# Kernel tuning notes

Measured on AMD Instinct MI355X. Metric: run time of the kernel, lower is better.

## Reference

```python
import jax, jax.numpy as jnp
import numpy as np

PI = 3.1415926
EPS_LN = 1e-5
SLOPE = 0.01  # nn.LeakyReLU default negative_slope


def _leaky(x):
    return jnp.where(x >= 0, x, SLOPE * x)


def _layernorm(x):
    # normalizes over dims (1,2) of [B,C,L], biased variance
    mean = x.mean(axis=(1, 2), keepdims=True)
    var = x.var(axis=(1, 2), keepdims=True)
    return (x - mean) / jnp.sqrt(var + EPS_LN)


def _conv1d(x, w, b):
    # x [B,C,L], w [O,I,3]
    y = jax.lax.conv_general_dilated(x, w, window_strides=(1,), padding='SAME',
                                     dimension_numbers=('NCH', 'OIH', 'NCH'))
    return y + b[None, :, None]


def _conv_stack(x, w1, b1, w2, b2, w3, b3):
    x = _leaky(_layernorm(_conv1d(x, w1, b1)))
    x = _leaky(_layernorm(_conv1d(x, w2, b2)))
    x = _leaky(_layernorm(_conv1d(x, w3, b3)))
    return x


def _context_pooling(feats, w1, b1, w2, b2, w3, b3, r=0.1):
    # feats [B,L,D]
    B, L, D = feats.shape
    sw = _conv_stack(feats.transpose(0, 2, 1), w1, b1, w2, b2, w3, b3)  # [B,2,L]
    s = jax.nn.softmax(sw[:, 0, :], axis=1)  # [B,L]
    w = jax.nn.softmax(sw[:, 1, :], axis=1)  # [B,L]
    std = r * L * s  # [B,L] (per query/center i)
    pos = jnp.arange(L, dtype=feats.dtype)
    diff2 = (pos[None, :] - pos[:, None]) ** 2  # [Li,Lj], (place - center)^2
    g = (2 * PI) ** -0.5 * (std[:, :, None] ** -1) * jnp.exp(
        -diff2[None] / (1e-5 + 2.0 * std[:, :, None] ** 2))  # [B,Li,Lj]
    g = g / jnp.max(g, axis=2, keepdims=True)
    W = g * w[:, None, :]  # [B,Li,Lj]
    return jnp.einsum('bij,bjd->bid', W, feats)


def setup_inputs() -> dict:
    key = jax.random.key(0)
    ks = jax.random.split(key, 16)
    B, L, D = 16, 1024, 640
    D2 = 2 * D
    f32 = jnp.float32
    sc = 0.02
    inp = {
        'feats': jax.random.normal(ks[0], (B, L, D), f32),
        # ContextPooling conv stack
        'cp_w1': jax.random.normal(ks[1], (D2, D, 3), f32) * sc,
        'cp_b1': jnp.zeros((D2,), f32),
        'cp_w2': jax.random.normal(ks[2], (D2, D2, 3), f32) * sc,
        'cp_b2': jnp.zeros((D2,), f32),
        'cp_w3': jax.random.normal(ks[3], (2, D2, 3), f32) * sc,
        'cp_b3': jnp.zeros((2,), f32),
        # SoluModel conv stack
        'cv_w1': jax.random.normal(ks[4], (D2, D, 3), f32) * sc,
        'cv_b1': jnp.zeros((D2,), f32),
        'cv_w2': jax.random.normal(ks[5], (D2, D2, 3), f32) * sc,
        'cv_b2': jnp.zeros((D2,), f32),
        'cv_w3': jax.random.normal(ks[6], (D, D2, 3), f32) * sc,
        'cv_b3': jnp.zeros((D,), f32),
        # MLP: Linear(2D -> D), torch init normal(0, 0.01), bias 0
        'mlp_w': jax.random.normal(ks[7], (D, 2 * D), f32) * 0.01,
        'mlp_b': jnp.zeros((D,), f32),
    }
    return inp


def reference(feats, cp_w1, cp_b1, cp_w2, cp_b2, cp_w3, cp_b3,
              cv_w1, cv_b1, cv_w2, cv_b2, cv_w3, cv_b3, mlp_w, mlp_b):
    out_sa = _context_pooling(feats, cp_w1, cp_b1, cp_w2, cp_b2, cp_w3, cp_b3) + feats
    out_conv = _conv_stack(feats.transpose(0, 2, 1),
                           cv_w1, cv_b1, cv_w2, cv_b2, cv_w3, cv_b3)
    out_conv = out_conv.transpose(0, 2, 1) + feats
    out = jnp.concatenate([out_sa, out_conv], axis=2)  # [B,L,2D]
    # Dropout(p=0.6) is identity at inference
    out = _leaky(jnp.einsum('bld,od->blo', out, mlp_w) + mlp_b)
    return out
```

## Files before the change

kernel.cpp:

```cpp
#include <hip/hip_runtime.h>
#include <hip/hip_bf16.h>
#include <math.h>

#define SLOPE 0.01f
#define EPS_LN 1e-5f

typedef __hip_bfloat16 bf16;
typedef __attribute__((ext_vector_type(8))) short short8;
typedef __attribute__((ext_vector_type(4))) float f32x4;

__device__ __forceinline__ float leakyf(float x) { return x < 0.f ? SLOPE * x : x; }

__device__ __forceinline__ float b2f(short s) {
    unsigned u = ((unsigned)(unsigned short)s) << 16;
    return __builtin_bit_cast(float, u);
}
__device__ __forceinline__ short f2b(float f) {
    __hip_bfloat16 h = __float2bfloat16(f);
    return *(short*)&h;
}

__device__ __forceinline__ void gload_lds16(const void* g, void* l) {
    __builtin_amdgcn_global_load_lds(
        (const __attribute__((address_space(1))) void*)g,
        (__attribute__((address_space(3))) void*)l, 16, 0, 0);
}

template <int EPI>
__global__ __launch_bounds__(256, 2) void gemm_bf16(
    const bf16* __restrict__ A, long sA, int ldA,
    const bf16* __restrict__ Bt,
    const float* __restrict__ bias,
    void* __restrict__ Outv, long sO, int ldO, int K,
    int gx, int gy, float2* __restrict__ stats)
{
    __shared__ bf16 As[128][64];
    __shared__ bf16 Bs[128][64];

    const int nwg = gridDim.x;
    const int wid = (blockIdx.x & 7) * (nwg >> 3) + (blockIdx.x >> 3);
    const int bx = wid % gx;
    const int by = (wid / gx) % gy;
    const int bz = wid / (gx * gy);

    const bf16* Ab = A + (long)bz * sA + (long)by * 128 * ldA;
    const bf16* Bb = Bt + (long)bx * 128 * K;
    const int tid = threadIdx.x;
    const int wave = tid >> 6, lane = tid & 63;
    const int moff = (wave >> 1) * 64, noff = (wave & 1) * 64;
    const int r16 = lane & 15, g4 = lane >> 4;
    const int r7 = r16 & 7;

    f32x4 acc[4][4];
#pragma unroll
    for (int i = 0; i < 4; ++i)
#pragma unroll
        for (int j = 0; j < 4; ++j)
            acc[i][j] = (f32x4){0.f, 0.f, 0.f, 0.f};

    for (int k0 = 0; k0 < K; k0 += 64) {
        __syncthreads();
#pragma unroll
        for (int i = 0; i < 4; ++i) {
            int chunk = i * 256 + tid;
            int row = chunk >> 3;
            int kc = (chunk ^ (chunk >> 3)) & 7;
            gload_lds16(Ab + (long)row * ldA + (k0 + kc * 8),
                        (char*)(&As[0][0]) + (i * 256 + wave * 64) * 16);
        }
#pragma unroll
        for (int i = 0; i < 4; ++i) {
            int chunk = i * 256 + tid;
            int row = chunk >> 3;
            int kc = (chunk ^ (chunk >> 3)) & 7;
            gload_lds16(Bb + (long)row * K + (k0 + kc * 8),
                        (char*)(&Bs[0][0]) + (i * 256 + wave * 64) * 16);
        }
        __syncthreads();
#pragma unroll
        for (int kk = 0; kk < 2; ++kk) {
            short8 af[4], bfr[4];
#pragma unroll
            for (int mi = 0; mi < 4; ++mi)
                af[mi] = *(const short8*)&As[moff + mi * 16 + r16][((kk * 4 + g4) ^ r7) * 8];
#pragma unroll
            for (int ni = 0; ni < 4; ++ni)
                bfr[ni] = *(const short8*)&Bs[noff + ni * 16 + r16][((kk * 4 + g4) ^ r7) * 8];
#pragma unroll
            for (int mi = 0; mi < 4; ++mi)
#pragma unroll
                for (int ni = 0; ni < 4; ++ni)
                    acc[mi][ni] = __builtin_amdgcn_mfma_f32_16x16x32_bf16(
                        af[mi], bfr[ni], acc[mi][ni], 0, 0, 0);
        }
    }

    float s = 0.f, q = 0.f;
#pragma unroll
    for (int mi = 0; mi < 4; ++mi) {
#pragma unroll
        for (int ni = 0; ni < 4; ++ni) {
            int col = bx * 128 + noff + ni * 16 + r16;
            float bv = bias[col];
#pragma unroll
            for (int r = 0; r < 4; ++r) {
                int row = by * 128 + moff + mi * 16 + g4 * 4 + r;
                float v = acc[mi][ni][r] + bv;
                if (EPI == 1) {
                    ((float*)Outv)[(long)bz * sO + (long)row * ldO + col] = leakyf(v);
                } else {
                    ((bf16*)Outv)[(long)bz * sO + (long)row * ldO + col] = __float2bfloat16(v);
                    s += v; q += v * v;
                }
            }
        }
    }
    if (EPI == 0) {
        __syncthreads();
        float* red = (float*)&As[0][0];
        float* red2 = red + 256;
        red[tid] = s; red2[tid] = q;
        __syncthreads();
        for (int o = 128; o; o >>= 1) {
            if (tid < o) { red[tid] += red[tid + o]; red2[tid] += red2[tid + o]; }
            __syncthreads();
        }
        if (tid == 0) {
            atomicAdd(&stats[bz].x, red[0]);
            atomicAdd(&stats[bz].y, red2[0]);
        }
    }
}

__global__ void zero_stats_k(float2* s) {
    if (threadIdx.x < 16) s[threadIdx.x] = make_float2(0.f, 0.f);
}

__global__ void fin_k(const float2* __restrict__ acc, float2* __restrict__ stat, float invN) {
    int b = threadIdx.x;
    if (b < 16) {
        float m = acc[b].x * invN;
        float var = acc[b].y * invN - m * m;
        stat[b] = make_float2(m, rsqrtf(var + EPS_LN));
    }
}

__global__ void pack_feats_v_k(const float* __restrict__ f, bf16* __restrict__ xp, int C)
{
    long i8 = (long)blockIdx.x * 256 + threadIdx.x;
    long total8 = 16L * 1026 * C / 8;
    if (i8 >= total8) return;
    long e = i8 * 8;
    int c = (int)(e % C);
    long t = e / C;
    int r = (int)(t % 1026);
    int b = (int)(t / 1026);
    short8 o;
    if (r == 0 || r == 1025) {
#pragma unroll
        for (int j = 0; j < 8; ++j) o[j] = 0;
    } else {
        const float* src = f + ((long)b * 1024 + (r - 1)) * C + c;
        f32x4 v0 = *(const f32x4*)src;
        f32x4 v1 = *(const f32x4*)(src + 4);
#pragma unroll
        for (int j = 0; j < 4; ++j) { o[j] = f2b(v0[j]); o[j + 4] = f2b(v1[j]); }
    }
    *(short8*)(xp + e) = o;
}

__global__ void norm_pack_v_k(const bf16* __restrict__ y, const float2* __restrict__ stat,
                              bf16* __restrict__ xp, int C)
{
    long i8 = (long)blockIdx.x * 256 + threadIdx.x;
    long total8 = 16L * 1026 * C / 8;
    if (i8 >= total8) return;
    long e = i8 * 8;
    int c = (int)(e % C);
    long t = e / C;
    int r = (int)(t % 1026);
    int b = (int)(t / 1026);
    short8 o;
    if (r == 0 || r == 1025) {
#pragma unroll
        for (int j = 0; j < 8; ++j) o[j] = 0;
    } else {
        float2 st = stat[b];
        short8 v = *(const short8*)(y + ((long)b * 1024 + (r - 1)) * C + c);
#pragma unroll
        for (int j = 0; j < 8; ++j)
            o[j] = f2b(leakyf((b2f(v[j]) - st.x) * st.y));
    }
    *(short8*)(xp + e) = o;
}

__global__ void norm_addf_v_k(const bf16* __restrict__ y, const float2* __restrict__ stat,
                              const float* __restrict__ feats, bf16* __restrict__ acat)
{
    long i8 = (long)blockIdx.x * 256 + threadIdx.x;
    long total8 = 16L * 1024 * 640 / 8;
    if (i8 >= total8) return;
    long e = i8 * 8;
    int c = (int)(e % 640);
    int l = (int)((e / 640) % 1024);
    int b = (int)(e / (640L * 1024));
    float2 st = stat[b];
    short8 v = *(const short8*)(y + e);
    f32x4 f0 = *(const f32x4*)(feats + e);
    f32x4 f1 = *(const f32x4*)(feats + e + 4);
    short8 o;
#pragma unroll
    for (int j = 0; j < 4; ++j) {
        o[j] = f2b(leakyf((b2f(v[j]) - st.x) * st.y) + f0[j]);
        o[j + 4] = f2b(leakyf((b2f(v[j + 4]) - st.x) * st.y) + f1[j]);
    }
    *(short8*)(acat + ((long)b * 1024 + l) * 1280 + 640 + c) = o;
}

__global__ void conv3cp_k(const bf16* __restrict__ xp, const bf16* __restrict__ w3,
                          const float* __restrict__ b3, float* __restrict__ sw)
{
    int wid = (int)((blockIdx.x * 256 + threadIdx.x) >> 6);
    int lane = threadIdx.x & 63;
    int b = wid >> 10, l = wid & 1023;
    const bf16* xr = xp + ((long)b * 1026 + l) * 1280;
    float a0 = 0.f, a1 = 0.f;
    for (int k = lane; k < 3840; k += 64) {
        float x = __bfloat162float(xr[k]);
        a0 += x * __bfloat162float(w3[k]);
        a1 += x * __bfloat162float(w3[3840 + k]);
    }
    for (int o = 32; o; o >>= 1) { a0 += __shfl_down(a0, o); a1 += __shfl_down(a1, o); }
    if (lane == 0) {
        sw[b * 2048 + l] = a0 + b3[0];
        sw[b * 2048 + 1024 + l] = a1 + b3[1];
    }
}

__global__ __launch_bounds__(256) void cp_post_k(const float* __restrict__ sw,
                                                 float* __restrict__ stdb,
                                                 float* __restrict__ wb)
{
    int b = blockIdx.x, tid = threadIdx.x;
    __shared__ float s0[1024], s1[1024], red[256];
    const float* p = sw + b * 2048;
    float s = 0.f, q = 0.f;
    for (int l = tid; l < 1024; l += 256) {
        float v0 = p[l], v1 = p[1024 + l];
        s0[l] = v0; s1[l] = v1;
        s += v0 + v1; q += v0 * v0 + v1 * v1;
    }
    red[tid] = s; __syncthreads();
    for (int o = 128; o; o >>= 1) { if (tid < o) red[tid] += red[tid + o]; __syncthreads(); }
    float mean = red[0] / 2048.f; __syncthreads();
    red[tid] = q; __syncthreads();
    for (int o = 128; o; o >>= 1) { if (tid < o) red[tid] += red[tid + o]; __syncthreads(); }
    float inv = rsqrtf(red[0] / 2048.f - mean * mean + EPS_LN); __syncthreads();
    for (int l = tid; l < 1024; l += 256) {
        s0[l] = leakyf((s0[l] - mean) * inv);
        s1[l] = leakyf((s1[l] - mean) * inv);
    }
    __syncthreads();
    float mx = -1e30f;
    for (int l = tid; l < 1024; l += 256) mx = fmaxf(mx, s0[l]);
    red[tid] = mx; __syncthreads();
    for (int o = 128; o; o >>= 1) { if (tid < o) red[tid] = fmaxf(red[tid], red[tid + o]); __syncthreads(); }
    mx = red[0]; __syncthreads();
    float se = 0.f;
    for (int l = tid; l < 1024; l += 256) { float e = __expf(s0[l] - mx); s0[l] = e; se += e; }
    red[tid] = se; __syncthreads();
    for (int o = 128; o; o >>= 1) { if (tid < o) red[tid] += red[tid + o]; __syncthreads(); }
    float rs = 1.f / red[0]; __syncthreads();
    for (int l = tid; l < 1024; l += 256) stdb[b * 1024 + l] = 102.4f * s0[l] * rs;
    mx = -1e30f;
    for (int l = tid; l < 1024; l += 256) mx = fmaxf(mx, s1[l]);
    red[tid] = mx; __syncthreads();
    for (int o = 128; o; o >>= 1) { if (tid < o) red[tid] = fmaxf(red[tid], red[tid + o]); __syncthreads(); }
    mx = red[0]; __syncthreads();
    se = 0.f;
    for (int l = tid; l < 1024; l += 256) { float e = __expf(s1[l] - mx); s1[l] = e; se += e; }
    red[tid] = se; __syncthreads();
    for (int o = 128; o; o >>= 1) { if (tid < o) red[tid] += red[tid + o]; __syncthreads(); }
    rs = 1.f / red[0]; __syncthreads();
    for (int l = tid; l < 1024; l += 256) wb[b * 1024 + l] = s1[l] * rs;
}

__global__ __launch_bounds__(256) void pool_k(const float* __restrict__ feats,
                                              const float* __restrict__ stdb,
                                              const float* __restrict__ wb,
                                              bf16* __restrict__ acat)
{
    int i = blockIdx.x, b = blockIdx.y, tid = threadIdx.x;
    float sd = stdb[b * 1024 + i];
    float den = 1e-5f + 2.f * sd * sd;
    float inv = 1.f / den;
    int R = (int)sqrtf(11.5129255f * den) + 1;
    int jlo = max(0, i - R), jhi = min(1023, i + R);
    __shared__ float cj[256];
    float a0 = 0.f, a1 = 0.f, a2 = 0.f;
    const float* fb = feats + (long)b * 1024 * 640;
    for (int j0 = jlo; j0 <= jhi; j0 += 256) {
        int j = j0 + tid;
        float c = 0.f;
        if (j <= jhi) {
            float d = (float)(j - i);
            c = __expf(-d * d * inv) * wb[b * 1024 + j];
        }
        __syncthreads();
        cj[tid] = c;
        __syncthreads();
        int lim = min(256, jhi - j0 + 1);
        for (int t = 0; t < lim; ++t) {
            float cc = cj[t];
            const float* fr = fb + (long)(j0 + t) * 640;
            a0 += cc * fr[tid];
            a1 += cc * fr[tid + 256];
            if (tid < 128) a2 += cc * fr[tid + 512];
        }
    }
    long obase = ((long)b * 1024 + i) * 1280;
    long fbase = ((long)b * 1024 + i) * 640;
    acat[obase + tid] = __float2bfloat16(a0 + feats[fbase + tid]);
    acat[obase + tid + 256] = __float2bfloat16(a1 + feats[fbase + tid + 256]);
    if (tid < 128) acat[obase + tid + 512] = __float2bfloat16(a2 + feats[fbase + tid + 512]);
}

__global__ void repack_w_k(const float* __restrict__ w, bf16* __restrict__ bt, int CO, int CI)
{
    long idx = (long)blockIdx.x * 256 + threadIdx.x;
    long total = (long)CO * CI * 3;
    if (idx >= total) return;
    int K3 = 3 * CI;
    int o = (int)(idx / K3);
    int k = (int)(idx % K3);
    int t = k / CI, ci = k % CI;
    bt[idx] = __float2bfloat16(w[(long)o * CI * 3 + ci * 3 + t]);
}

__global__ void cast_bf16_k(const float* __restrict__ w, bf16* __restrict__ o, long n)
{
    long idx = (long)blockIdx.x * 256 + threadIdx.x;
    if (idx < n) o[idx] = __float2bfloat16(w[idx]);
}

extern "C" void kernel_launch(void* const* d_in, const int* in_sizes, int n_in,
                              void* d_out, int out_size, void* d_ws, size_t ws_size,
                              hipStream_t stream)
{
    const float* feats = (const float*)d_in[0];
    const float* cp_w1 = (const float*)d_in[1];
    const float* cp_b1 = (const float*)d_in[2];
    const float* cp_w2 = (const float*)d_in[3];
    const float* cp_b2 = (const float*)d_in[4];
    const float* cp_w3 = (const float*)d_in[5];
    const float* cp_b3 = (const float*)d_in[6];
    const float* cv_w1 = (const float*)d_in[7];
    const float* cv_b1 = (const float*)d_in[8];
    const float* cv_w2 = (const float*)d_in[9];
    const float* cv_b2 = (const float*)d_in[10];
    const float* cv_w3 = (const float*)d_in[11];
    const float* cv_b3 = (const float*)d_in[12];
    const float* mlp_w = (const float*)d_in[13];
    const float* mlp_b = (const float*)d_in[14];
    float* out = (float*)d_out;

    char* ws = (char*)d_ws;
    size_t off = 0;
    auto alloc = [&](size_t bytes) -> char* {
        char* p = ws + off;
        off += (bytes + 255) & ~(size_t)255;
        return p;
    };
    bf16* XpadF = (bf16*)alloc(16L * 1026 * 640 * 2);
    bf16* Xpad2 = (bf16*)alloc(16L * 1026 * 1280 * 2);
    bf16* Ybf = (bf16*)alloc(16L * 1024 * 1280 * 2);
    bf16* Acat = (bf16*)alloc(16L * 1024 * 1280 * 2);
    bf16* Bcp1 = (bf16*)alloc(1280L * 1920 * 2);
    bf16* Bcp2 = (bf16*)alloc(1280L * 3840 * 2);
    bf16* Bcp3 = (bf16*)alloc(2L * 3840 * 2);
    bf16* Bcv1 = (bf16*)alloc(1280L * 1920 * 2);
    bf16* Bcv2 = (bf16*)alloc(1280L * 3840 * 2);
    bf16* Bcv3 = (bf16*)alloc(640L * 3840 * 2);
    bf16* Bmlp = (bf16*)alloc(640L * 1280 * 2);
    float* swb = (float*)alloc(16L * 2048 * 4);
    float* stdb = (float*)alloc(16L * 1024 * 4);
    float* wbf = (float*)alloc(16L * 1024 * 4);
    float2* sacc = (float2*)alloc(16L * 8);
    float2* stat = (float2*)alloc(16L * 8);
    (void)ws_size; (void)in_sizes; (void)n_in; (void)out_size;

    const long NF8 = 16L * 1026 * 640 / 8;
    const long N28 = 16L * 1026 * 1280 / 8;
    const long NA8 = 16L * 1024 * 640 / 8;
    const long N1280 = 1024L * 1280, N640 = 1024L * 640;
    const float inv1280 = 1.f / (float)N1280, inv640 = 1.f / (float)N640;

    pack_feats_v_k<<<(NF8 + 255) / 256, 256, 0, stream>>>(feats, XpadF, 640);
    repack_w_k<<<(1280L * 640 * 3 + 255) / 256, 256, 0, stream>>>(cp_w1, Bcp1, 1280, 640);
    repack_w_k<<<(1280L * 1280 * 3 + 255) / 256, 256, 0, stream>>>(cp_w2, Bcp2, 1280, 1280);
    repack_w_k<<<(2L * 1280 * 3 + 255) / 256, 256, 0, stream>>>(cp_w3, Bcp3, 2, 1280);
    repack_w_k<<<(1280L * 640 * 3 + 255) / 256, 256, 0, stream>>>(cv_w1, Bcv1, 1280, 640);
    repack_w_k<<<(1280L * 1280 * 3 + 255) / 256, 256, 0, stream>>>(cv_w2, Bcv2, 1280, 1280);
    repack_w_k<<<(640L * 1280 * 3 + 255) / 256, 256, 0, stream>>>(cv_w3, Bcv3, 640, 1280);
    cast_bf16_k<<<(640L * 1280 + 255) / 256, 256, 0, stream>>>(mlp_w, Bmlp, 640L * 1280);

    zero_stats_k<<<1, 64, 0, stream>>>(sacc);
    gemm_bf16<0><<<1280, 256, 0, stream>>>(XpadF, 1026L * 640, 640, Bcp1, cp_b1,
                                           Ybf, N1280, 1280, 1920, 10, 8, sacc);
    fin_k<<<1, 64, 0, stream>>>(sacc, stat, inv1280);
    norm_pack_v_k<<<(N28 + 255) / 256, 256, 0, stream>>>(Ybf, stat, Xpad2, 1280);
    zero_stats_k<<<1, 64, 0, stream>>>(sacc);
    gemm_bf16<0><<<1280, 256, 0, stream>>>(Xpad2, 1026L * 1280, 1280, Bcp2, cp_b2,
                                           Ybf, N1280, 1280, 3840, 10, 8, sacc);
    fin_k<<<1, 64, 0, stream>>>(sacc, stat, inv1280);
    norm_pack_v_k<<<(N28 + 255) / 256, 256, 0, stream>>>(Ybf, stat, Xpad2, 1280);
    conv3cp_k<<<4096, 256, 0, stream>>>(Xpad2, Bcp3, cp_b3, swb);
    cp_post_k<<<16, 256, 0, stream>>>(swb, stdb, wbf);
    pool_k<<<dim3(1024, 16), 256, 0, stream>>>(feats, stdb, wbf, Acat);

    zero_stats_k<<<1, 64, 0, stream>>>(sacc);
    gemm_bf16<0><<<1280, 256, 0, stream>>>(XpadF, 1026L * 640, 640, Bcv1, cv_b1,
                                           Ybf, N1280, 1280, 1920, 10, 8, sacc);
    fin_k<<<1, 64, 0, stream>>>(sacc, stat, inv1280);
    norm_pack_v_k<<<(N28 + 255) / 256, 256, 0, stream>>>(Ybf, stat, Xpad2, 1280);
    zero_stats_k<<<1, 64, 0, stream>>>(sacc);
    gemm_bf16<0><<<1280, 256, 0, stream>>>(Xpad2, 1026L * 1280, 1280, Bcv2, cv_b2,
                                           Ybf, N1280, 1280, 3840, 10, 8, sacc);
    fin_k<<<1, 64, 0, stream>>>(sacc, stat, inv1280);
    norm_pack_v_k<<<(N28 + 255) / 256, 256, 0, stream>>>(Ybf, stat, Xpad2, 1280);
    zero_stats_k<<<1, 64, 0, stream>>>(sacc);
    gemm_bf16<0><<<640, 256, 0, stream>>>(Xpad2, 1026L * 1280, 1280, Bcv3, cv_b3,
                                          Ybf, N640, 640, 3840, 5, 8, sacc);
    fin_k<<<1, 64, 0, stream>>>(sacc, stat, inv640);
    norm_addf_v_k<<<(NA8 + 255) / 256, 256, 0, stream>>>(Ybf, stat, feats, Acat);

    gemm_bf16<1><<<640, 256, 0, stream>>>(Acat, N1280, 1280, Bmlp, mlp_b,
                                          out, N640, 640, 1280, 5, 8, nullptr);
}
```

Measured before the change: 855.3 us.

## Batch paired conv-stack GEMMs into a 256x256-tile 8-wave pipelined kernel

Adds a new 512-thread GEMM kernel with 256x256 tiles, four-slot LDS ring buffering via direct global-to-LDS loads, XOR-swizzled LDS layout, and explicit barrier/priority scheduling around MFMA phases. The ContextPooling and conv-stack first and second layers, which share shapes, now run as single launches covering both branches, each keeping its own stats slots. This removes launch and tail overhead and gives larger tiles more operand reuse. It also vectorizes the conv3cp dot product with 16-byte loads and aliases workspace buffers. The cost is more buffers, heavy register use at one block per CU, and dependence on hand-tuned waitcnt counts.

```diff
diff --git a/kernel.cpp b/kernel.cpp
--- a/kernel.cpp
+++ b/kernel.cpp
@@ -24,6 +24,162 @@
     __builtin_amdgcn_global_load_lds(
         (const __attribute__((address_space(1))) void*)g,
         (__attribute__((address_space(3))) void*)l, 16, 0, 0);
+}
+
+#define PHASE_MFMA(NFB)                                                        \
+    asm volatile("s_barrier" ::: "memory");                                    \
+    asm volatile("s_waitcnt lgkmcnt(0)" ::: "memory");                         \
+    __builtin_amdgcn_sched_barrier(0);                                         \
+    __builtin_amdgcn_s_setprio(1);                                             \
+    _Pragma("unroll")                                                          \
+    for (int mi = 0; mi < 8; ++mi) {                                           \
+        acc[mi][NFB] = __builtin_amdgcn_mfma_f32_16x16x32_bf16(                \
+            areg[mi], b0, acc[mi][NFB], 0, 0, 0);                              \
+        acc[mi][NFB + 1] = __builtin_amdgcn_mfma_f32_16x16x32_bf16(            \
+            areg[mi], b1, acc[mi][NFB + 1], 0, 0, 0);                          \
+    }                                                                          \
+    __builtin_amdgcn_s_setprio(0);
+
+template <int MODE>
+__global__ __launch_bounds__(512, 1) void gemm8_bf16(
+    const bf16* __restrict__ A0, const bf16* __restrict__ A1,
+    const bf16* __restrict__ Bt0, const bf16* __restrict__ Bt1,
+    const float* __restrict__ bias0, const float* __restrict__ bias1,
+    bf16* __restrict__ Y0, bf16* __restrict__ Y1,
+    float2* __restrict__ sacc)
+{
+    constexpr int K   = (MODE == 0) ? 1920 : 3840;
+    constexpr int LDA = (MODE == 0) ? 640 : 1280;
+    constexpr int MT  = (MODE == 0) ? 64 : 128;
+    constexpr int NKT = K / 64;
+
+    __shared__ bf16 Ash[4][256][32];
+    __shared__ bf16 Bsh[4][256][32];
+
+    const int nwg = gridDim.x;
+    const int wid = (blockIdx.x & 7) * (nwg >> 3) + (blockIdx.x >> 3);
+    const int mt = wid % MT;
+    const int bxg = wid / MT;
+    int branch, bxl, mtl;
+    if (MODE == 0) { branch = bxg >= 5; bxl = bxg - branch * 5; mtl = mt; }
+    else           { branch = mt >= 64; bxl = bxg; mtl = mt & 63; }
+    const int batch = mtl >> 2;
+    const int mrow0 = (mtl & 3) * 256;
+    const bf16* Apad = branch ? A1 : A0;
+    const bf16* Bt   = branch ? Bt1 : Bt0;
+    const float* bias = branch ? bias1 : bias0;
+    bf16* Yb = branch ? Y1 : Y0;
+    const bf16* Abase = Apad + ((long)batch * 1026 + mrow0) * LDA;
+    const bf16* Bbase = Bt + (long)bxl * 256 * K;
+
+    const int tid = threadIdx.x;
+    const int wave = tid >> 6, lane = tid & 63;
+    const int wm = wave >> 2, wn = wave & 3;
+    const int r16 = lane & 15, g4 = lane >> 4;
+
+    auto stageA = [&](int s, int kh) {
+        char* lb = (char*)&Ash[(2 * s + kh) & 3][0][0];
+#pragma unroll
+        for (int j = 0; j < 2; ++j) {
+            int c = j * 512 + tid;
+            int L = c ^ ((c >> 3) & 7);
+            int row = L >> 2, kg = L & 3;
+            gload_lds16(Abase + (long)row * LDA + (s * 64 + kh * 32 + kg * 8),
+                        lb + c * 16);
+        }
+    };
+    auto stageB = [&](int s, int kh) {
+        char* lb = (char*)&Bsh[(2 * s + kh) & 3][0][0];
+#pragma unroll
+        for (int j = 0; j < 2; ++j) {
+            int c = j * 512 + tid;
+            int L = c ^ ((c >> 3) & 7);
+            int row = L >> 2, kg = L & 3;
+            gload_lds16(Bbase + (long)row * K + (s * 64 + kh * 32 + kg * 8),
+                        lb + c * 16);
+        }
+    };
+    auto ldA8 = [&](int reg, int mi) -> short8 {
+        int row = wm * 128 + mi * 16 + r16;
+        int P = ((row << 2) | g4) ^ ((row >> 1) & 7);
+        return *(const short8*)((const char*)&Ash[reg][0][0] + P * 16);
+    };
+    auto ldB8 = [&](int reg, int q) -> short8 {
+        int row = wn * 64 + q * 16 + r16;
+        int P = ((row << 2) | g4) ^ ((row >> 1) & 7);
+        return *(const short8*)((const char*)&Bsh[reg][0][0] + P * 16);
+    };
+
+    f32x4 acc[8][4];
+#pragma unroll
+    for (int i = 0; i < 8; ++i)
+#pragma unroll
+        for (int j = 0; j < 4; ++j) acc[i][j] = (f32x4){0.f, 0.f, 0.f, 0.f};
+
+    stageA(0, 0); stageB(0, 0);
+    stageA(0, 1); stageB(0, 1);
+    stageA(1, 0); stageB(1, 0);
+    asm volatile("s_waitcnt vmcnt(8)" ::: "memory");
+    asm volatile("s_barrier" ::: "memory");
+
+    short8 areg[8];
+    short8 b0, b1;
+    for (int s = 0; s < NKT; ++s) {
+        const int rA = (2 * s) & 3;
+        const int rB = (2 * s + 1) & 3;
+#pragma unroll
+        for (int mi = 0; mi < 8; ++mi) areg[mi] = ldA8(rA, mi);
+        b0 = ldB8(rA, 0); b1 = ldB8(rA, 1);
+        if (s + 1 < NKT) stageA(s + 1, 1);
+        PHASE_MFMA(0)
+        asm volatile("s_barrier" ::: "memory");
+        b0 = ldB8(rA, 2); b1 = ldB8(rA, 3);
+        if (s + 1 < NKT) stageB(s + 1, 1);
+        PHASE_MFMA(2)
+        asm volatile("s_waitcnt vmcnt(8)" ::: "memory");
+        asm volatile("s_barrier" ::: "memory");
+#pragma unroll
+        for (int mi = 0; mi < 8; ++mi) areg[mi] = ldA8(rB, mi);
+        b0 = ldB8(rB, 0); b1 = ldB8(rB, 1);
+        if (s + 2 < NKT) stageA(s + 2, 0);
+        PHASE_MFMA(0)
+        asm volatile("s_barrier" ::: "memory");
+        b0 = ldB8(rB, 2); b1 = ldB8(rB, 3);
+        if (s + 2 < NKT) stageB(s + 2, 0);
+        PHASE_MFMA(2)
+        asm volatile("s_waitcnt vmcnt(8)" ::: "memory");
+        asm volatile("s_barrier" ::: "memory");
+    }
+    asm volatile("s_waitcnt vmcnt(0) lgkmcnt(0)" ::: "memory");
+
+    float ssum = 0.f, sq = 0.f;
+#pragma unroll
+    for (int mi = 0; mi < 8; ++mi) {
+#pragma unroll
+        for (int q = 0; q < 4; ++q) {
+            int col = bxl * 256 + wn * 64 + q * 16 + r16;
+            float bv = bias[col];
+#pragma unroll
+            for (int rr = 0; rr < 4; ++rr) {
+                int row = mrow0 + wm * 128 + mi * 16 + g4 * 4 + rr;
+                float v = acc[mi][q][rr] + bv;
+                Yb[((long)batch * 1024 + row) * 1280 + col] = __float2bfloat16(v);
+                ssum += v; sq += v * v;
+            }
+        }
+    }
+    __syncthreads();
+    float* red = (float*)&Ash[0][0][0];
+    red[tid] = ssum; red[512 + tid] = sq;
+    __syncthreads();
+    for (int o = 256; o; o >>= 1) {
+        if (tid < o) { red[tid] += red[tid + o]; red[512 + tid] += red[512 + tid + o]; }
+        __syncthreads();
+    }
+    if (tid == 0) {
+        atomicAdd(&sacc[branch * 16 + batch].x, red[0]);
+        atomicAdd(&sacc[branch * 16 + batch].y, red[512]);
+    }
 }
 
 template <int EPI>
@@ -133,12 +289,13 @@
 }
 
 __global__ void zero_stats_k(float2* s) {
-    if (threadIdx.x < 16) s[threadIdx.x] = make_float2(0.f, 0.f);
-}
-
-__global__ void fin_k(const float2* __restrict__ acc, float2* __restrict__ stat, float invN) {
+    if (threadIdx.x < 80) s[threadIdx.x] = make_float2(0.f, 0.f);
+}
+
+__global__ void fin_k(const float2* __restrict__ acc, float2* __restrict__ stat,
+                      float invN, int n) {
     int b = threadIdx.x;
-    if (b < 16) {
+    if (b < n) {
         float m = acc[b].x * invN;
         float var = acc[b].y * invN - m * m;
         stat[b] = make_float2(m, rsqrtf(var + EPS_LN));
@@ -223,12 +380,18 @@
     int wid = (int)((blockIdx.x * 256 + threadIdx.x) >> 6);
     int lane = threadIdx.x & 63;
     int b = wid >> 10, l = wid & 1023;
-    const bf16* xr = xp + ((long)b * 1026 + l) * 1280;
+    const short8* xr = (const short8*)(xp + ((long)b * 1026 + l) * 1280);
+    const short8* w0 = (const short8*)w3;
+    const short8* w1 = (const short8*)(w3 + 3840);
     float a0 = 0.f, a1 = 0.f;
-    for (int k = lane; k < 3840; k += 64) {
-        float x = __bfloat162float(xr[k]);
-        a0 += x * __bfloat162float(w3[k]);
-        a1 += x * __bfloat162float(w3[3840 + k]);
+    for (int c = lane; c < 480; c += 64) {
+        short8 x = xr[c], u = w0[c], v = w1[c];
+#pragma unroll
+        for (int j = 0; j < 8; ++j) {
+            float xf = b2f(x[j]);
+            a0 += xf * b2f(u[j]);
+            a1 += xf * b2f(v[j]);
+        }
     }
     for (int o = 32; o; o >>= 1) { a0 += __shfl_down(a0, o); a1 += __shfl_down(a1, o); }
     if (lane == 0) {
@@ -371,22 +534,25 @@
         off += (bytes + 255) & ~(size_t)255;
         return p;
     };
-    bf16* XpadF = (bf16*)alloc(16L * 1026 * 640 * 2);
-    bf16* Xpad2 = (bf16*)alloc(16L * 1026 * 1280 * 2);
-    bf16* Ybf = (bf16*)alloc(16L * 1024 * 1280 * 2);
-    bf16* Acat = (bf16*)alloc(16L * 1024 * 1280 * 2);
-    bf16* Bcp1 = (bf16*)alloc(1280L * 1920 * 2);
+    char* R1 = alloc(16L * 1024 * 1280 * 2);
+    bf16* XpadF = (bf16*)R1;
+    bf16* Acat = (bf16*)R1;
+    bf16* Xp_cp = (bf16*)alloc(16L * 1026 * 1280 * 2);
+    bf16* Xp_cv = (bf16*)alloc(16L * 1026 * 1280 * 2);
+    bf16* Y0 = (bf16*)alloc(16L * 1024 * 1280 * 2);
+    bf16* Y1 = (bf16*)alloc(16L * 1024 * 1280 * 2);
+    bf16* Ycv3 = Y0;
+    bf16* Bm1 = (bf16*)alloc(2560L * 1920 * 2);
     bf16* Bcp2 = (bf16*)alloc(1280L * 3840 * 2);
+    bf16* Bcv2 = (bf16*)alloc(1280L * 3840 * 2);
     bf16* Bcp3 = (bf16*)alloc(2L * 3840 * 2);
-    bf16* Bcv1 = (bf16*)alloc(1280L * 1920 * 2);
-    bf16* Bcv2 = (bf16*)alloc(1280L * 3840 * 2);
     bf16* Bcv3 = (bf16*)alloc(640L * 3840 * 2);
     bf16* Bmlp = (bf16*)alloc(640L * 1280 * 2);
     float* swb = (float*)alloc(16L * 2048 * 4);
     float* stdb = (float*)alloc(16L * 1024 * 4);
     float* wbf = (float*)alloc(16L * 1024 * 4);
-    float2* sacc = (float2*)alloc(16L * 8);
-    float2* stat = (float2*)alloc(16L * 8);
+    float2* sacc = (float2*)alloc(80L * 8);
+    float2* stat = (float2*)alloc(80L * 8);
     (void)ws_size; (void)in_sizes; (void)n_in; (void)out_size;
 
     const long NF8 = 16L * 1026 * 640 / 8;
@@ -395,44 +561,36 @@
     const long N1280 = 1024L * 1280, N640 = 1024L * 640;
     const float inv1280 = 1.f / (float)N1280, inv640 = 1.f / (float)N640;
 
+    zero_stats_k<<<1, 128, 0, stream>>>(sacc);
     pack_feats_v_k<<<(NF8 + 255) / 256, 256, 0, stream>>>(feats, XpadF, 640);
-    repack_w_k<<<(1280L * 640 * 3 + 255) / 256, 256, 0, stream>>>(cp_w1, Bcp1, 1280, 640);
+    repack_w_k<<<(1280L * 640 * 3 + 255) / 256, 256, 0, stream>>>(cp_w1, Bm1, 1280, 640);
+    repack_w_k<<<(1280L * 640 * 3 + 255) / 256, 256, 0, stream>>>(cv_w1, Bm1 + 1280L * 1920, 1280, 640);
     repack_w_k<<<(1280L * 1280 * 3 + 255) / 256, 256, 0, stream>>>(cp_w2, Bcp2, 1280, 1280);
+    repack_w_k<<<(1280L * 1280 * 3 + 255) / 256, 256, 0, stream>>>(cv_w2, Bcv2, 1280, 1280);
     repack_w_k<<<(2L * 1280 * 3 + 255) / 256, 256, 0, stream>>>(cp_w3, Bcp3, 2, 1280);
-    repack_w_k<<<(1280L * 640 * 3 + 255) / 256, 256, 0, stream>>>(cv_w1, Bcv1, 1280, 640);
-    repack_w_k<<<(1280L * 1280 * 3 + 255) / 256, 256, 0, stream>>>(cv_w2, Bcv2, 1280, 1280);
     repack_w_k<<<(640L * 1280 * 3 + 255) / 256, 256, 0, stream>>>(cv_w3, Bcv3, 640, 1280);
     cast_bf16_k<<<(640L * 1280 + 255) / 256, 256, 0, stream>>>(mlp_w, Bmlp, 640L * 1280);
 
-    zero_stats_k<<<1, 64, 0, stream>>>(sacc);
-    gemm_bf16<0><<<1280, 256, 0, stream>>>(XpadF, 1026L * 640, 640, Bcp1, cp_b1,
-                                           Ybf, N1280, 1280, 1920, 10, 8, sacc);
-    fin_k<<<1, 64, 0, stream>>>(sacc, stat, inv1280);
-    norm_pack_v_k<<<(N28 + 255) / 256, 256, 0, stream>>>(Ybf, stat, Xpad2, 1280);
-    zero_stats_k<<<1, 64, 0, stream>>>(sacc);
-    gemm_bf16<0><<<1280, 256, 0, stream>>>(Xpad2, 1026L * 1280, 1280, Bcp2, cp_b2,
-                                           Ybf, N1280, 1280, 3840, 10, 8, sacc);
-    fin_k<<<1, 64, 0, stream>>>(sacc, stat, inv1280);
-    norm_pack_v_k<<<(N28 + 255) / 256, 256, 0, stream>>>(Ybf, stat, Xpad2, 1280);
-    conv3cp_k<<<4096, 256, 0, stream>>>(Xpad2, Bcp3, cp_b3, swb);
+    gemm8_bf16<0><<<640, 512, 0, stream>>>(XpadF, XpadF, Bm1, Bm1 + 1280L * 1920,
+                                           cp_b1, cv_b1, Y0, Y1, sacc);
+    fin_k<<<1, 64, 0, stream>>>(sacc, stat, inv1280, 32);
+    norm_pack_v_k<<<(N28 + 255) / 256, 256, 0, stream>>>(Y0, stat, Xp_cp, 1280);
+    norm_pack_v_k<<<(N28 + 255) / 256, 256, 0, stream>>>(Y1, stat + 16, Xp_cv, 1280);
+
+    gemm8_bf16<1><<<640, 512, 0, stream>>>(Xp_cp, Xp_cv, Bcp2, Bcv2,
+                                           cp_b2, cv_b2, Y0, Y1, sacc + 32);
+    fin_k<<<1, 64, 0, stream>>>(sacc + 32, stat + 32, inv1280, 32);
+    norm_pack_v_k<<<(N28 + 255) / 256, 256, 0, stream>>>(Y0, stat + 32, Xp_cp, 1280);
+    norm_pack_v_k<<<(N28 + 255) / 256, 256, 0, stream>>>(Y1, stat + 48, Xp_cv, 1280);
+
+    conv3cp_k<<<4096, 256, 0, stream>>>(Xp_cp, Bcp3, cp_b3, swb);
     cp_post_k<<<16, 256, 0, stream>>>(swb, stdb, wbf);
     pool_k<<<dim3(1024, 16), 256, 0, stream>>>(feats, stdb, wbf, Acat);
 
-    zero_stats_k<<<1, 64, 0, stream>>>(sacc);
-    gemm_bf16<0><<<1280, 256, 0, stream>>>(XpadF, 1026L * 640, 640, Bcv1, cv_b1,
-                                           Ybf, N1280, 1280, 1920, 10, 8, sacc);
-    fin_k<<<1, 64, 0, stream>>>(sacc, stat, inv1280);
-    norm_pack_v_k<<<(N28 + 255) / 256, 256, 0, stream>>>(Ybf, stat, Xpad2, 1280);
-    zero_stats_k<<<1, 64, 0, stream>>>(sacc);
-    gemm_bf16<0><<<1280, 256, 0, stream>>>(Xpad2, 1026L * 1280, 1280, Bcv2, cv_b2,
-                                           Ybf, N1280, 1280, 3840, 10, 8, sacc);
-    fin_k<<<1, 64, 0, stream>>>(sacc, stat, inv1280);
-    norm_pack_v_k<<<(N28 + 255) / 256, 256, 0, stream>>>(Ybf, stat, Xpad2, 1280);
-    zero_stats_k<<<1, 64, 0, stream>>>(sacc);
-    gemm_bf16<0><<<640, 256, 0, stream>>>(Xpad2, 1026L * 1280, 1280, Bcv3, cv_b3,
-                                          Ybf, N640, 640, 3840, 5, 8, sacc);
-    fin_k<<<1, 64, 0, stream>>>(sacc, stat, inv640);
-    norm_addf_v_k<<<(NA8 + 255) / 256, 256, 0, stream>>>(Ybf, stat, feats, Acat);
+    gemm_bf16<0><<<640, 256, 0, stream>>>(Xp_cv, 1026L * 1280, 1280, Bcv3, cv_b3,
+                                          Ycv3, N640, 640, 3840, 5, 8, sacc + 64);
+    fin_k<<<1, 64, 0, stream>>>(sacc + 64, stat + 64, inv640, 16);
+    norm_addf_v_k<<<(NA8 + 255) / 256, 256, 0, stream>>>(Ycv3, stat + 64, feats, Acat);
 
     gemm_bf16<1><<<640, 256, 0, stream>>>(Acat, N1280, 1280, Bmlp, mlp_b,
                                           out, N640, 640, 1280, 5, 8, nullptr);
```

Measured after the change: 910.1 us. +6.4%, slower.

## Batch context-pooling and conv branches into dual GEMM launches

Applied to the files above, without the earlier changes.

Merges the matching layer-1 and layer-2 convolution GEMMs of the two branches into single launches with twice the workgroups. Each workgroup picks its branch pointers, and each branch gets separate stats slots, all zeroed once. The workspace is reorganised so both branches keep their own intermediate buffers, and the input pack buffer is aliased with the concat buffer. Separately, the final 2-channel conv is vectorised to 16-byte loads. This targets launch overhead and wave tail inefficiency, at the cost of more workspace.

```diff
diff --git a/kernel.cpp b/kernel.cpp
--- a/kernel.cpp
+++ b/kernel.cpp
@@ -27,21 +27,30 @@
 }
 
 template <int EPI>
-__global__ __launch_bounds__(256, 2) void gemm_bf16(
-    const bf16* __restrict__ A, long sA, int ldA,
-    const bf16* __restrict__ Bt,
-    const float* __restrict__ bias,
-    void* __restrict__ Outv, long sO, int ldO, int K,
-    int gx, int gy, float2* __restrict__ stats)
+__global__ __launch_bounds__(256, 2) void gemm_dual(
+    const bf16* __restrict__ A0, const bf16* __restrict__ A1, long sA, int ldA,
+    const bf16* __restrict__ Bt0, const bf16* __restrict__ Bt1,
+    const float* __restrict__ bias0, const float* __restrict__ bias1,
+    void* __restrict__ Out0, void* __restrict__ Out1, long sO, int ldO, int K,
+    int gx, int gy, int halfwg,
+    float2* __restrict__ stats0, float2* __restrict__ stats1)
 {
     __shared__ bf16 As[128][64];
     __shared__ bf16 Bs[128][64];
 
     const int nwg = gridDim.x;
     const int wid = (blockIdx.x & 7) * (nwg >> 3) + (blockIdx.x >> 3);
-    const int bx = wid % gx;
-    const int by = (wid / gx) % gy;
-    const int bz = wid / (gx * gy);
+    const int branch = wid >= halfwg;
+    const int w = wid - branch * halfwg;
+    const int bx = w % gx;
+    const int by = (w / gx) % gy;
+    const int bz = w / (gx * gy);
+
+    const bf16* A = branch ? A1 : A0;
+    const bf16* Bt = branch ? Bt1 : Bt0;
+    const float* bias = branch ? bias1 : bias0;
+    void* Outv = branch ? Out1 : Out0;
+    float2* stats = branch ? stats1 : stats0;
 
     const bf16* Ab = A + (long)bz * sA + (long)by * 128 * ldA;
     const bf16* Bb = Bt + (long)bx * 128 * K;
@@ -133,12 +142,13 @@
 }
 
 __global__ void zero_stats_k(float2* s) {
-    if (threadIdx.x < 16) s[threadIdx.x] = make_float2(0.f, 0.f);
-}
-
-__global__ void fin_k(const float2* __restrict__ acc, float2* __restrict__ stat, float invN) {
+    if (threadIdx.x < 80) s[threadIdx.x] = make_float2(0.f, 0.f);
+}
+
+__global__ void fin_k(const float2* __restrict__ acc, float2* __restrict__ stat,
+                      float invN, int n) {
     int b = threadIdx.x;
-    if (b < 16) {
+    if (b < n) {
         float m = acc[b].x * invN;
         float var = acc[b].y * invN - m * m;
         stat[b] = make_float2(m, rsqrtf(var + EPS_LN));
@@ -223,12 +233,18 @@
     int wid = (int)((blockIdx.x * 256 + threadIdx.x) >> 6);
     int lane = threadIdx.x & 63;
     int b = wid >> 10, l = wid & 1023;
-    const bf16* xr = xp + ((long)b * 1026 + l) * 1280;
+    const short8* xr = (const short8*)(xp + ((long)b * 1026 + l) * 1280);
+    const short8* w0 = (const short8*)w3;
+    const short8* w1 = (const short8*)(w3 + 3840);
     float a0 = 0.f, a1 = 0.f;
-    for (int k = lane; k < 3840; k += 64) {
-        float x = __bfloat162float(xr[k]);
-        a0 += x * __bfloat162float(w3[k]);
-        a1 += x * __bfloat162float(w3[3840 + k]);
+    for (int c = lane; c < 480; c += 64) {
+        short8 x = xr[c], u = w0[c], v = w1[c];
+#pragma unroll
+        for (int j = 0; j < 8; ++j) {
+            float xf = b2f(x[j]);
+            a0 += xf * b2f(u[j]);
+            a1 += xf * b2f(v[j]);
+        }
     }
     for (int o = 32; o; o >>= 1) { a0 += __shfl_down(a0, o); a1 += __shfl_down(a1, o); }
     if (lane == 0) {
@@ -371,22 +387,25 @@
         off += (bytes + 255) & ~(size_t)255;
         return p;
     };
-    bf16* XpadF = (bf16*)alloc(16L * 1026 * 640 * 2);
-    bf16* Xpad2 = (bf16*)alloc(16L * 1026 * 1280 * 2);
-    bf16* Ybf = (bf16*)alloc(16L * 1024 * 1280 * 2);
-    bf16* Acat = (bf16*)alloc(16L * 1024 * 1280 * 2);
-    bf16* Bcp1 = (bf16*)alloc(1280L * 1920 * 2);
+    char* R1 = alloc(16L * 1024 * 1280 * 2);
+    bf16* XpadF = (bf16*)R1;
+    bf16* Acat = (bf16*)R1;
+    bf16* Xp_cp = (bf16*)alloc(16L * 1026 * 1280 * 2);
+    bf16* Xp_cv = (bf16*)alloc(16L * 1026 * 1280 * 2);
+    bf16* Y0 = (bf16*)alloc(16L * 1024 * 1280 * 2);
+    bf16* Y1 = (bf16*)alloc(16L * 1024 * 1280 * 2);
+    bf16* Ycv3 = Y0;
+    bf16* Bm1 = (bf16*)alloc(2560L * 1920 * 2);
     bf16* Bcp2 = (bf16*)alloc(1280L * 3840 * 2);
+    bf16* Bcv2 = (bf16*)alloc(1280L * 3840 * 2);
     bf16* Bcp3 = (bf16*)alloc(2L * 3840 * 2);
-    bf16* Bcv1 = (bf16*)alloc(1280L * 1920 * 2);
-    bf16* Bcv2 = (bf16*)alloc(1280L * 3840 * 2);
     bf16* Bcv3 = (bf16*)alloc(640L * 3840 * 2);
     bf16* Bmlp = (bf16*)alloc(640L * 1280 * 2);
     float* swb = (float*)alloc(16L * 2048 * 4);
     float* stdb = (float*)alloc(16L * 1024 * 4);
     float* wbf = (float*)alloc(16L * 1024 * 4);
-    float2* sacc = (float2*)alloc(16L * 8);
-    float2* stat = (float2*)alloc(16L * 8);
+    float2* sacc = (float2*)alloc(80L * 8);
+    float2* stat = (float2*)alloc(80L * 8);
     (void)ws_size; (void)in_sizes; (void)n_in; (void)out_size;
 
     const long NF8 = 16L * 1026 * 640 / 8;
@@ -395,45 +414,45 @@
     const long N1280 = 1024L * 1280, N640 = 1024L * 640;
     const float inv1280 = 1.f / (float)N1280, inv640 = 1.f / (float)N640;
 
+    zero_stats_k<<<1, 128, 0, stream>>>(sacc);
     pack_feats_v_k<<<(NF8 + 255) / 256, 256, 0, stream>>>(feats, XpadF, 640);
-    repack_w_k<<<(1280L * 640 * 3 + 255) / 256, 256, 0, stream>>>(cp_w1, Bcp1, 1280, 640);
+    repack_w_k<<<(1280L * 640 * 3 + 255) / 256, 256, 0, stream>>>(cp_w1, Bm1, 1280, 640);
+    repack_w_k<<<(1280L * 640 * 3 + 255) / 256, 256, 0, stream>>>(cv_w1, Bm1 + 1280L * 1920, 1280, 640);
     repack_w_k<<<(1280L * 1280 * 3 + 255) / 256, 256, 0, stream>>>(cp_w2, Bcp2, 1280, 1280);
+    repack_w_k<<<(1280L * 1280 * 3 + 255) / 256, 256, 0, stream>>>(cv_w2, Bcv2, 1280, 1280);
     repack_w_k<<<(2L * 1280 * 3 + 255) / 256, 256, 0, stream>>>(cp_w3, Bcp3, 2, 1280);
-    repack_w_k<<<(1280L * 640 * 3 + 255) / 256, 256, 0, stream>>>(cv_w1, Bcv1, 1280, 640);
-    repack_w_k<<<(1280L * 1280 * 3 + 255) / 256, 256, 0, stream>>>(cv_w2, Bcv2, 1280, 1280);
     repack_w_k<<<(640L * 1280 * 3 + 255) / 256, 256, 0, stream>>>(cv_w3, Bcv3, 640, 1280);
     cast_bf16_k<<<(640L * 1280 + 255) / 256, 256, 0, stream>>>(mlp_w, Bmlp, 640L * 1280);
 
-    zero_stats_k<<<1, 64, 0, stream>>>(sacc);
-    gemm_bf16<0><<<1280, 256, 0, stream>>>(XpadF, 1026L * 640, 640, Bcp1, cp_b1,
-                                           Ybf, N1280, 1280, 1920, 10, 8, sacc);
-    fin_k<<<1, 64, 0, stream>>>(sacc, stat, inv1280);
-    norm_pack_v_k<<<(N28 + 255) / 256, 256, 0, stream>>>(Ybf, stat, Xpad2, 1280);
-    zero_stats_k<<<1, 64, 0, stream>>>(sacc);
-    gemm_bf16<0><<<1280, 256, 0, stream>>>(Xpad2, 1026L * 1280, 1280, Bcp2, cp_b2,
-                                           Ybf, N1280, 1280, 3840, 10, 8, sacc);
-    fin_k<<<1, 64, 0, stream>>>(sacc, stat, inv1280);
-    norm_pack_v_k<<<(N28 + 255) / 256, 256, 0, stream>>>(Ybf, stat, Xpad2, 1280);
-    conv3cp_k<<<4096, 256, 0, stream>>>(Xpad2, Bcp3, cp_b3, swb);
+    gemm_dual<0><<<2560, 256, 0, stream>>>(
+        XpadF, XpadF, 1026L * 640, 640, Bm1, Bm1 + 1280L * 1920,
+        cp_b1, cv_b1, Y0, Y1, N1280, 1280, 1920, 10, 8, 1280,
+        sacc, sacc + 16);
+    fin_k<<<1, 64, 0, stream>>>(sacc, stat, inv1280, 32);
+    norm_pack_v_k<<<(N28 + 255) / 256, 256, 0, stream>>>(Y0, stat, Xp_cp, 1280);
+    norm_pack_v_k<<<(N28 + 255) / 256, 256, 0, stream>>>(Y1, stat + 16, Xp_cv, 1280);
+
+    gemm_dual<0><<<2560, 256, 0, stream>>>(
+        Xp_cp, Xp_cv, 1026L * 1280, 1280, Bcp2, Bcv2,
+        cp_b2, cv_b2, Y0, Y1, N1280, 1280, 3840, 10, 8, 1280,
+        sacc + 32, sacc + 48);
+    fin_k<<<1, 64, 0, stream>>>(sacc + 32, stat + 32, inv1280, 32);
+    norm_pack_v_k<<<(N28 + 255) / 256, 256, 0, stream>>>(Y0, stat + 32, Xp_cp, 1280);
+    norm_pack_v_k<<<(N28 + 255) / 256, 256, 0, stream>>>(Y1, stat + 48, Xp_cv, 1280);
+
+    conv3cp_k<<<4096, 256, 0, stream>>>(Xp_cp, Bcp3, cp_b3, swb);
     cp_post_k<<<16, 256, 0, stream>>>(swb, stdb, wbf);
     pool_k<<<dim3(1024, 16), 256, 0, stream>>>(feats, stdb, wbf, Acat);
 
-    zero_stats_k<<<1, 64, 0, stream>>>(sacc);
-    gemm_bf16<0><<<1280, 256, 0, stream>>>(XpadF, 1026L * 640, 640, Bcv1, cv_b1,
-                                           Ybf, N1280, 1280, 1920, 10, 8, sacc);
-    fin_k<<<1, 64, 0, stream>>>(sacc, stat, inv1280);
-    norm_pack_v_k<<<(N28 + 255) / 256, 256, 0, stream>>>(Ybf, stat, Xpad2, 1280);
-    zero_stats_k<<<1, 64, 0, stream>>>(sacc);
-    gemm_bf16<0><<<1280, 256, 0, stream>>>(Xpad2, 1026L * 1280, 1280, Bcv2, cv_b2,
-                                           Ybf, N1280, 1280, 3840, 10, 8, sacc);
-    fin_k<<<1, 64, 0, stream>>>(sacc, stat, inv1280);
-    norm_pack_v_k<<<(N28 + 255) / 256, 256, 0, stream>>>(Ybf, stat, Xpad2, 1280);
-    zero_stats_k<<<1, 64, 0, stream>>>(sacc);
-    gemm_bf16<0><<<640, 256, 0, stream>>>(Xpad2, 1026L * 1280, 1280, Bcv3, cv_b3,
-                                          Ybf, N640, 640, 3840, 5, 8, sacc);
-    fin_k<<<1, 64, 0, stream>>>(sacc, stat, inv640);
-    norm_addf_v_k<<<(NA8 + 255) / 256, 256, 0, stream>>>(Ybf, stat, feats, Acat);
-
-    gemm_bf16<1><<<640, 256, 0, stream>>>(Acat, N1280, 1280, Bmlp, mlp_b,
-                                          out, N640, 640, 1280, 5, 8, nullptr);
-}
+    gemm_dual<0><<<640, 256, 0, stream>>>(
+        Xp_cv, Xp_cv, 1026L * 1280, 1280, Bcv3, Bcv3,
+        cv_b3, cv_b3, Ycv3, Ycv3, N640, 640, 3840, 5, 8, 640,
+        sacc + 64, sacc + 64);
+    fin_k<<<1, 64, 0, stream>>>(sacc + 64, stat + 64, inv640, 16);
+    norm_addf_v_k<<<(NA8 + 255) / 256, 256, 0, stream>>>(Ycv3, stat + 64, feats, Acat);
+
+    gemm_dual<1><<<640, 256, 0, stream>>>(
+        Acat, Acat, N1280, 1280, Bmlp, Bmlp,
+        mlp_b, mlp_b, out, out, N640, 640, 1280, 5, 8, 640,
+        nullptr, nullptr);
+}
```

Measured after the change: 787.3 us. 1.09x faster.
